# Optimization experiments

Measured on AMD Instinct MI355X. Metric: run time of the kernel, lower is better.

Reference implementation:

```python
import jax, jax.numpy as jnp
import numpy as np

N_NODES = 100000
N_EDGES = 1250000
IN_CH = 64
HID = 64
OUT = 64


def setup_inputs() -> dict:
    key = jax.random.key(0)
    ks = jax.random.split(key, 8)
    x = jax.random.normal(ks[0], (N_NODES, IN_CH), dtype=jnp.float32)
    edge_index = jax.random.randint(ks[1], (2, N_EDGES), 0, N_NODES, dtype=jnp.int64)
    # glorot-ish init for weights, zeros for biases (PyG GCNConv default-style)
    def glorot(k, fan_in, fan_out):
        s = (6.0 / (fan_in + fan_out)) ** 0.5
        return jax.random.uniform(k, (fan_in, fan_out), jnp.float32, -s, s)
    W1 = glorot(ks[2], IN_CH, HID)
    b1 = jnp.zeros((HID,), jnp.float32)
    W2 = glorot(ks[3], HID, HID)
    b2 = jnp.zeros((HID,), jnp.float32)
    W3 = glorot(ks[4], HID, OUT)
    b3 = jnp.zeros((OUT,), jnp.float32)
    return {"x": x, "edge_index": edge_index, "W1": W1, "b1": b1,
            "W2": W2, "b2": b2, "W3": W3, "b3": b3}


def _gcn_conv(x, src, dst, W, b, n_nodes):
    """PyG GCNConv: out = D^{-1/2} (A + I) D^{-1/2} (x W) + b.
    src/dst already include self-loops."""
    deg = jax.ops.segment_sum(jnp.ones_like(dst, dtype=x.dtype), dst,
                              num_segments=n_nodes)  # in-degree incl. self-loop
    dinv = jnp.where(deg > 0, jax.lax.rsqrt(deg), 0.0)
    norm = dinv[src] * dinv[dst]                       # [E+N]
    h = x @ W                                          # [N, F_out] small GEMM
    msg = h[src] * norm[:, None]                       # gather + scale (edge-wise)
    out = jax.ops.segment_sum(msg, dst, num_segments=n_nodes)  # scatter-add
    return out + b


def reference(x, edge_index, W1, b1, W2, b2, W3, b3):
    n_nodes = x.shape[0]
    loop = jnp.arange(n_nodes, dtype=edge_index.dtype)
    src = jnp.concatenate([edge_index[0], loop])  # messages flow src -> dst
    dst = jnp.concatenate([edge_index[1], loop])
    h = jax.nn.relu(_gcn_conv(x, src, dst, W1, b1, n_nodes))
    h = jax.nn.relu(_gcn_conv(h, src, dst, W2, b2, n_nodes))
    return h @ W3 + b3
```

## Files before the change

### kernel.cpp

```cpp
#include <hip/hip_runtime.h>
#include <hip/hip_bf16.h>


#define WG 256
#define BSHIFT 9
#define BSIZE  (1 << BSHIFT)
#define BCAP   8192
#define PCHUNK 2048
#define WT_LD  72

typedef __attribute__((ext_vector_type(8))) short bf16x8;
typedef __attribute__((ext_vector_type(4))) float f32x4;

__device__ __forceinline__ unsigned short f2bf(float f) {
    union { float f; unsigned u; } v; v.f = f;
    unsigned r = v.u + 0x7fffu + ((v.u >> 16) & 1u);
    return (unsigned short)(r >> 16);
}
__device__ __forceinline__ float bf2f(unsigned short h) {
    union { unsigned u; float f; } v; v.u = ((unsigned)h) << 16;
    return v.f;
}

__global__ __launch_bounds__(WG) void bcur_init(int* __restrict__ cur2, int nbk) {
    int b = threadIdx.x;
    if (b < nbk) cur2[b] = b * BCAP;
}

__global__ __launch_bounds__(WG) void partition(const int* __restrict__ ei,
                                                int* __restrict__ cur2,
                                                unsigned long long* __restrict__ pairs,
                                                int E) {
    __shared__ int hist[256];
    __shared__ int gbase[256];
    __shared__ int lb[256];
    __shared__ int sums[WG];
    __shared__ unsigned long long sp[PCHUNK];
    __shared__ int sd[PCHUNK];
    const int t = threadIdx.x;
    const int base = blockIdx.x * PCHUNK;
    const int total = min(PCHUNK, E - base);

    hist[t] = 0;
    __syncthreads();

    int s[8], d[8], r[8];
#pragma unroll
    for (int i = 0; i < 8; i++) {
        int e = base + i * WG + t;
        bool ok = e < E;
        s[i] = ok ? ei[e] : 0;
        d[i] = ok ? ei[E + e] : 0;
        r[i] = ok ? atomicAdd(&hist[d[i] >> BSHIFT], 1) : 0;
        if (!ok) d[i] = -1;
    }
    __syncthreads();

    int hv = hist[t];
    if (hv > 0) gbase[t] = atomicAdd(&cur2[t], hv);
    sums[t] = hv;
    __syncthreads();
    for (int ofs = 1; ofs < WG; ofs <<= 1) {
        int u = (t >= ofs) ? sums[t - ofs] : 0;
        __syncthreads();
        sums[t] += u;
        __syncthreads();
    }
    lb[t] = sums[t] - hv;
    __syncthreads();

#pragma unroll
    for (int i = 0; i < 8; i++) {
        if (d[i] >= 0) {
            int b = d[i] >> BSHIFT;
            int slot = lb[b] + r[i];
            sp[slot] = ((unsigned long long)(unsigned)(d[i] & (BSIZE - 1)) << 32) |
                       (unsigned)s[i];
            sd[slot] = gbase[b] + r[i];
        }
    }
    __syncthreads();

    for (int j = t; j < total; j += WG)
        pairs[sd[j]] = sp[j];
}

__global__ __launch_bounds__(WG) void bsum_scan(const int* __restrict__ cur2,
                                                int* __restrict__ bbase, int nbk,
                                                int* __restrict__ off, int N) {
    __shared__ int sums[WG];
    const int t = threadIdx.x;
    int s = (t < nbk) ? (cur2[t] - t * BCAP) : 0;
    sums[t] = s;
    __syncthreads();
    for (int ofs = 1; ofs < WG; ofs <<= 1) {
        int u = (t >= ofs) ? sums[t - ofs] : 0;
        __syncthreads();
        sums[t] += u;
        __syncthreads();
    }
    if (t < nbk) bbase[t] = sums[t] - s;
    if (t == WG - 1) off[N] = sums[WG - 1];
}

__global__ __launch_bounds__(1024) void csr_local(const unsigned long long* __restrict__ pairs,
                                                  const int* __restrict__ cur2,
                                                  const int* __restrict__ bbase,
                                                  int* __restrict__ off,
                                                  float* __restrict__ dinv,
                                                  int* __restrict__ csr, int N) {
    __shared__ int h[BSIZE];
    __shared__ int cur[BSIZE];
    __shared__ int sums[1024];
    const int b = blockIdx.x;
    const int t = threadIdx.x;
    const int node0 = b << BSHIFT;
    const int nlocal = min(BSIZE, N - node0);
    const int pstart = b * BCAP;
    const int pend = cur2[b];
    const int base = bbase[b];

    if (t < BSIZE) h[t] = 0;
    __syncthreads();

    for (int e = pstart + t; e < pend; e += 1024)
        atomicAdd(&h[(int)(pairs[e] >> 32)], 1);
    __syncthreads();

    int s = (t < BSIZE) ? h[t] : 0;
    sums[t] = s;
    __syncthreads();
    for (int ofs = 1; ofs < 1024; ofs <<= 1) {
        int u = (t >= ofs) ? sums[t - ofs] : 0;
        __syncthreads();
        sums[t] += u;
        __syncthreads();
    }
    if (t < nlocal) {
        int run = base + sums[t] - s;
        off[node0 + t] = run;
        cur[t] = run;
        dinv[node0 + t] = rsqrtf((float)(s + 1));
    }
    __syncthreads();

    for (int e = pstart + t; e < pend; e += 1024) {
        unsigned long long p = pairs[e];
        int local = (int)(p >> 32);
        int src = (int)(p & 0xffffffffu);
        int pos = atomicAdd(&cur[local], 1);
        csr[pos] = src;
    }
}

__global__ __launch_bounds__(WG, 4) void gemm_fused(
    const float* __restrict__ in, const float* __restrict__ W,
    const float* __restrict__ dinv, const float* __restrict__ b_pre, int pre_flag,
    int post_scale, const float* __restrict__ b_post,
    void* __restrict__ out1, int out_bf16, int n_rows)
{
    __shared__ __align__(16) short Wh[64 * WT_LD];
    __shared__ __align__(16) short Wl[64 * WT_LD];

    const int t = threadIdx.x;

    const float4* W4 = (const float4*)W;
#pragma unroll
    for (int i = 0; i < 4; i++) {
        int q = i * WG + t;
        float4 w = W4[q];
        int base = q * 4;
        int k = base >> 6;
        int j0 = base & 63;
        float wf[4] = {w.x, w.y, w.z, w.w};
#pragma unroll
        for (int e = 0; e < 4; e++) {
            unsigned short h = f2bf(wf[e]);
            Wh[(j0 + e) * WT_LD + k] = (short)h;
            Wl[(j0 + e) * WT_LD + k] = (short)f2bf(wf[e] - bf2f(h));
        }
    }

    const int wid = t >> 6;
    const int l = t & 63;
    const int lr = l & 15;
    const int lk = l >> 4;
    const int row0 = blockIdx.x * 64 + wid * 16;
    const int arow = row0 + lr;
    const int srow = (arow < n_rows) ? arow : 0;

    bf16x8 ah[2], al[2];
    float dv = pre_flag ? dinv[srow] : 0.f;
#pragma unroll
    for (int kc = 0; kc < 2; kc++) {
        const float* p = in + (size_t)srow * 64 + kc * 32 + lk * 8;
        float4 v0 = *(const float4*)p;
        float4 v1 = *(const float4*)(p + 4);
        float vv[8] = {v0.x, v0.y, v0.z, v0.w, v1.x, v1.y, v1.z, v1.w};
        if (pre_flag) {
            const float* bp = b_pre + kc * 32 + lk * 8;
            float4 b0 = *(const float4*)bp;
            float4 b1 = *(const float4*)(bp + 4);
            float bb[8] = {b0.x, b0.y, b0.z, b0.w, b1.x, b1.y, b1.z, b1.w};
#pragma unroll
            for (int e = 0; e < 8; e++)
                vv[e] = fmaxf(fmaf(dv, vv[e], bb[e]), 0.f);
        }
#pragma unroll
        for (int e = 0; e < 8; e++) {
            unsigned short h = f2bf(vv[e]);
            ah[kc][e] = (short)h;
            al[kc][e] = (short)f2bf(vv[e] - bf2f(h));
        }
    }

    __syncthreads();

    f32x4 acc[4] = {};
#pragma unroll
    for (int ct = 0; ct < 4; ct++) {
#pragma unroll
        for (int kc = 0; kc < 2; kc++) {
            const short* ph = &Wh[(ct * 16 + lr) * WT_LD + kc * 32 + lk * 8];
            const short* pl = &Wl[(ct * 16 + lr) * WT_LD + kc * 32 + lk * 8];
            bf16x8 bh = *(const bf16x8*)ph;
            bf16x8 bl = *(const bf16x8*)pl;
            acc[ct] = __builtin_amdgcn_mfma_f32_16x16x32_bf16(ah[kc], bh, acc[ct], 0, 0, 0);
            acc[ct] = __builtin_amdgcn_mfma_f32_16x16x32_bf16(al[kc], bh, acc[ct], 0, 0, 0);
            acc[ct] = __builtin_amdgcn_mfma_f32_16x16x32_bf16(ah[kc], bl, acc[ct], 0, 0, 0);
            acc[ct] = __builtin_amdgcn_mfma_f32_16x16x32_bf16(al[kc], bl, acc[ct], 0, 0, 0);
        }
    }

#pragma unroll
    for (int r = 0; r < 4; r++) {
        int orow = row0 + lk * 4 + r;
        if (orow >= n_rows) continue;
        float sc = post_scale ? dinv[orow] : 1.0f;
#pragma unroll
        for (int ct = 0; ct < 4; ct++) {
            float bpv = b_post ? b_post[ct * 16 + lr] : 0.f;
            float o = fmaf(acc[ct][r], sc, bpv);
            if (out_bf16)
                ((unsigned short*)out1)[((size_t)orow << 6) + ct * 16 + lr] = f2bf(o);
            else
                ((float*)out1)[((size_t)orow << 6) + ct * 16 + lr] = o;
        }
    }
}

__device__ __forceinline__ void acc_bf16x2(float& a, float& b, unsigned u) {
    union { unsigned v; float f; } lo, hi;
    lo.v = u << 16;
    hi.v = u & 0xffff0000u;
    a += lo.f;
    b += hi.f;
}

__global__ __launch_bounds__(WG) void aggregate(
    const uint2* __restrict__ A4, float* __restrict__ B,
    const int* __restrict__ off, const int* __restrict__ csr, int N)
{
    int node = blockIdx.x * 4 + (threadIdx.x >> 6);
    if (node >= N) return;
    const int l = threadIdx.x & 63;
    const int c = l & 15;
    const int g = l >> 4;

    const int s0 = off[node];
    const int s1 = off[node + 1];

    float4 acc = make_float4(0.f, 0.f, 0.f, 0.f);
    if (g == 0) {
        uint2 v = A4[((size_t)node << 4) + c];
        acc_bf16x2(acc.x, acc.y, v.x);
        acc_bf16x2(acc.z, acc.w, v.y);
    }

    for (int p = s0; p < s1; p += 64) {
        int cnt = min(64, s1 - p);
        int idx = (l < cnt) ? csr[p + l] : 0;
        for (int j = 0; j < cnt; j += 16) {
#pragma unroll
            for (int k = 0; k < 4; k++) {
                int e = j + 4 * g + k;
                int src = __shfl(idx, e);
                if (e < cnt) {
                    uint2 v = A4[((size_t)src << 4) + c];
                    acc_bf16x2(acc.x, acc.y, v.x);
                    acc_bf16x2(acc.z, acc.w, v.y);
                }
            }
        }
    }

    acc.x += __shfl_xor(acc.x, 16);
    acc.y += __shfl_xor(acc.y, 16);
    acc.z += __shfl_xor(acc.z, 16);
    acc.w += __shfl_xor(acc.w, 16);
    acc.x += __shfl_xor(acc.x, 32);
    acc.y += __shfl_xor(acc.y, 32);
    acc.z += __shfl_xor(acc.z, 32);
    acc.w += __shfl_xor(acc.w, 32);
    if (g == 0)
        *(float4*)(B + ((size_t)node << 6) + 4 * c) = acc;
}

extern "C" void kernel_launch(void* const* d_in, const int* in_sizes, int n_in,
                              void* d_out, int out_size, void* d_ws, size_t ws_size,
                              hipStream_t stream) {
    const float* x  = (const float*)d_in[0];
    const int*   ei = (const int*)d_in[1];
    const float* W1 = (const float*)d_in[2];
    const float* b1 = (const float*)d_in[3];
    const float* W2 = (const float*)d_in[4];
    const float* b2 = (const float*)d_in[5];
    const float* W3 = (const float*)d_in[6];
    const float* b3 = (const float*)d_in[7];
    float* out = (float*)d_out;

    const int N = in_sizes[0] / 64;
    const int E = in_sizes[1] / 2;
    const int nbk = (N + BSIZE - 1) / BSIZE;

    int*   off  = (int*)d_ws;
    int*   csr  = off + (N + 1);
    int*   cur2 = csr + E;
    int*   bbase= cur2 + 256;
    uintptr_t pa = (uintptr_t)(bbase + 256);
    pa = (pa + 255) & ~(uintptr_t)255;
    float* dinv = (float*)pa;
    __hip_bfloat16* A = (__hip_bfloat16*)(dinv + N);
    float* B    = (float*)(A + (size_t)N * 64);
    unsigned long long* pairs = (unsigned long long*)B;

    const int gG = (N + 63) / 64;
    const int gA = (N + 3) / 4;
    const int gP = (E + PCHUNK - 1) / PCHUNK;

    bcur_init<<<1,   WG, 0, stream>>>(cur2, nbk);
    partition<<<gP,  WG, 0, stream>>>(ei, cur2, pairs, E);
    bsum_scan<<<1,   WG, 0, stream>>>(cur2, bbase, nbk, off, N);
    csr_local<<<nbk, 1024, 0, stream>>>(pairs, cur2, bbase, off, dinv, csr, N);

    gemm_fused<<<gG, WG, 0, stream>>>(x, W1, dinv, nullptr, 0, 1, nullptr, A, 1, N);
    aggregate <<<gA, WG, 0, stream>>>((const uint2*)A, B, off, csr, N);

    gemm_fused<<<gG, WG, 0, stream>>>(B, W2, dinv, b1, 1, 1, nullptr, A, 1, N);
    aggregate <<<gA, WG, 0, stream>>>((const uint2*)A, B, off, csr, N);

    gemm_fused<<<gG, WG, 0, stream>>>(B, W3, dinv, b2, 1, 0, b3, out, 0, N);
}
```

Measured before the change: 253.4 us.

## Map one node per 16-lane group in aggregate and stage CSR build in LDS

```diff
diff --git a/kernel.cpp b/kernel.cpp
--- a/kernel.cpp
+++ b/kernel.cpp
@@ -34,10 +34,12 @@
     __shared__ int hist[256];
     __shared__ int gbase[256];
     __shared__ int lb[256];
-    __shared__ int sums[WG];
+    __shared__ int wsum4[4];
     __shared__ unsigned long long sp[PCHUNK];
     __shared__ int sd[PCHUNK];
     const int t = threadIdx.x;
+    const int lane = t & 63;
+    const int w = t >> 6;
     const int base = blockIdx.x * PCHUNK;
     const int total = min(PCHUNK, E - base);
 
@@ -58,15 +60,21 @@
 
     int hv = hist[t];
     if (hv > 0) gbase[t] = atomicAdd(&cur2[t], hv);
-    sums[t] = hv;
-    __syncthreads();
-    for (int ofs = 1; ofs < WG; ofs <<= 1) {
-        int u = (t >= ofs) ? sums[t - ofs] : 0;
-        __syncthreads();
-        sums[t] += u;
-        __syncthreads();
-    }
-    lb[t] = sums[t] - hv;
+    int sc = hv;
+#pragma unroll
+    for (int ofs = 1; ofs < 64; ofs <<= 1) {
+        int u = __shfl_up(sc, ofs);
+        if (lane >= ofs) sc += u;
+    }
+    if (lane == 63) wsum4[w] = sc;
+    __syncthreads();
+    if (t == 0) {
+        int run = 0;
+#pragma unroll
+        for (int i = 0; i < 4; i++) { int x = wsum4[i]; wsum4[i] = run; run += x; }
+    }
+    __syncthreads();
+    lb[t] = sc + wsum4[w] - hv;
     __syncthreads();
 
 #pragma unroll
@@ -109,48 +117,65 @@
                                                   int* __restrict__ off,
                                                   float* __restrict__ dinv,
                                                   int* __restrict__ csr, int N) {
+    __shared__ unsigned long long sp[BCAP];
+    __shared__ int cs[BCAP];
     __shared__ int h[BSIZE];
     __shared__ int cur[BSIZE];
-    __shared__ int sums[1024];
+    __shared__ int wsum[8];
     const int b = blockIdx.x;
     const int t = threadIdx.x;
+    const int lane = t & 63;
+    const int w = t >> 6;
     const int node0 = b << BSHIFT;
     const int nlocal = min(BSIZE, N - node0);
     const int pstart = b * BCAP;
-    const int pend = cur2[b];
+    const int cnt = cur2[b] - pstart;
     const int base = bbase[b];
 
     if (t < BSIZE) h[t] = 0;
     __syncthreads();
 
-    for (int e = pstart + t; e < pend; e += 1024)
-        atomicAdd(&h[(int)(pairs[e] >> 32)], 1);
-    __syncthreads();
-
-    int s = (t < BSIZE) ? h[t] : 0;
-    sums[t] = s;
-    __syncthreads();
-    for (int ofs = 1; ofs < 1024; ofs <<= 1) {
-        int u = (t >= ofs) ? sums[t - ofs] : 0;
-        __syncthreads();
-        sums[t] += u;
-        __syncthreads();
-    }
-    if (t < nlocal) {
-        int run = base + sums[t] - s;
-        off[node0 + t] = run;
-        cur[t] = run;
-        dinv[node0 + t] = rsqrtf((float)(s + 1));
-    }
-    __syncthreads();
-
-    for (int e = pstart + t; e < pend; e += 1024) {
-        unsigned long long p = pairs[e];
-        int local = (int)(p >> 32);
-        int src = (int)(p & 0xffffffffu);
-        int pos = atomicAdd(&cur[local], 1);
-        csr[pos] = src;
-    }
+    for (int e = t; e < cnt; e += 1024) {
+        unsigned long long p = pairs[pstart + e];
+        sp[e] = p;
+        atomicAdd(&h[(int)(p >> 32)], 1);
+    }
+    __syncthreads();
+
+    int myh = (t < BSIZE) ? h[t] : 0;
+    int s = myh;
+#pragma unroll
+    for (int d = 1; d < 64; d <<= 1) {
+        int u = __shfl_up(s, d);
+        if (lane >= d) s += u;
+    }
+    if (t < BSIZE && lane == 63) wsum[w] = s;
+    __syncthreads();
+    if (t == 0) {
+        int run = 0;
+#pragma unroll
+        for (int i = 0; i < 8; i++) { int x = wsum[i]; wsum[i] = run; run += x; }
+    }
+    __syncthreads();
+    if (t < BSIZE) {
+        int excl = s + wsum[w] - myh;
+        cur[t] = excl;
+        if (t < nlocal) {
+            off[node0 + t] = base + excl;
+            dinv[node0 + t] = rsqrtf((float)(myh + 1));
+        }
+    }
+    __syncthreads();
+
+    for (int e = t; e < cnt; e += 1024) {
+        unsigned long long p = sp[e];
+        int pos = atomicAdd(&cur[(int)(p >> 32)], 1);
+        cs[pos] = (int)(p & 0xffffffffu);
+    }
+    __syncthreads();
+
+    for (int j = t; j < cnt; j += 1024)
+        csr[base + j] = cs[j];
 }
 
 __global__ __launch_bounds__(WG, 4) void gemm_fused(
@@ -261,48 +286,38 @@
     const uint2* __restrict__ A4, float* __restrict__ B,
     const int* __restrict__ off, const int* __restrict__ csr, int N)
 {
-    int node = blockIdx.x * 4 + (threadIdx.x >> 6);
-    if (node >= N) return;
-    const int l = threadIdx.x & 63;
+    const int t = threadIdx.x;
+    const int l = t & 63;
     const int c = l & 15;
     const int g = l >> 4;
+    const int gl = g << 4;
+    int node = blockIdx.x * 16 + ((t >> 6) << 2) + g;
+    const bool valid = node < N;
+    if (!valid) node = N - 1;
 
     const int s0 = off[node];
-    const int s1 = off[node + 1];
-
+    const int s1 = valid ? off[node + 1] : s0;
+
+    uint2 v = A4[((size_t)node << 4) + c];
     float4 acc = make_float4(0.f, 0.f, 0.f, 0.f);
-    if (g == 0) {
-        uint2 v = A4[((size_t)node << 4) + c];
-        acc_bf16x2(acc.x, acc.y, v.x);
-        acc_bf16x2(acc.z, acc.w, v.y);
-    }
-
-    for (int p = s0; p < s1; p += 64) {
-        int cnt = min(64, s1 - p);
-        int idx = (l < cnt) ? csr[p + l] : 0;
-        for (int j = 0; j < cnt; j += 16) {
-#pragma unroll
-            for (int k = 0; k < 4; k++) {
-                int e = j + 4 * g + k;
-                int src = __shfl(idx, e);
-                if (e < cnt) {
-                    uint2 v = A4[((size_t)src << 4) + c];
-                    acc_bf16x2(acc.x, acc.y, v.x);
-                    acc_bf16x2(acc.z, acc.w, v.y);
-                }
+    acc_bf16x2(acc.x, acc.y, v.x);
+    acc_bf16x2(acc.z, acc.w, v.y);
+
+    for (int p = s0; p < s1; p += 16) {
+        const int cnt = min(16, s1 - p);
+        int idx = (c < cnt) ? csr[p + c] : 0;
+#pragma unroll
+        for (int k = 0; k < 16; k++) {
+            int src = __shfl(idx, gl + k);
+            if (k < cnt) {
+                uint2 wv = A4[((size_t)src << 4) + c];
+                acc_bf16x2(acc.x, acc.y, wv.x);
+                acc_bf16x2(acc.z, acc.w, wv.y);
             }
         }
     }
 
-    acc.x += __shfl_xor(acc.x, 16);
-    acc.y += __shfl_xor(acc.y, 16);
-    acc.z += __shfl_xor(acc.z, 16);
-    acc.w += __shfl_xor(acc.w, 16);
-    acc.x += __shfl_xor(acc.x, 32);
-    acc.y += __shfl_xor(acc.y, 32);
-    acc.z += __shfl_xor(acc.z, 32);
-    acc.w += __shfl_xor(acc.w, 32);
-    if (g == 0)
+    if (valid)
         *(float4*)(B + ((size_t)node << 6) + 4 * c) = acc;
 }
 
@@ -335,7 +350,7 @@
     unsigned long long* pairs = (unsigned long long*)B;
 
     const int gG = (N + 63) / 64;
-    const int gA = (N + 3) / 4;
+    const int gA = (N + 15) / 16;
     const int gP = (E + PCHUNK - 1) / PCHUNK;
 
     bcur_init<<<1,   WG, 0, stream>>>(cur2, nbk);
```

Result: faster. 232.8 us (-8.1%).
